# Performance work log

Hardware: AMD Instinct MI355X
Metric: run time of the kernel (lower is better)

## Reference

```python
import jax, jax.numpy as jnp
import numpy as np

N, E, G = 10000, 40000, 128          # nodes, edges, graphs
NF, EF, H, NH, GD, L = 92, 50, 64, 10, 108, 5  # feat dims, hidden, heads, global dim, layers
EPS = 1e-5

def _lrelu(v):
    return jax.nn.leaky_relu(v, 0.2)

def setup_inputs() -> dict:
    key = jax.random.key(0)
    ks = jax.random.split(key, 24)
    def rn(k, shp, s=0.05):
        return jax.random.normal(k, shp, jnp.float32) * s
    return {
        "x": jax.random.normal(ks[0], (N, NF), jnp.float32),
        "edge_index": jax.random.randint(ks[1], (2, E), 0, N, dtype=jnp.int32),
        "edge_attr": jax.random.normal(ks[2], (E, EF), jnp.float32),
        "batch_idx": jnp.sort(jax.random.randint(ks[3], (N,), 0, G, dtype=jnp.int32)),
        "global_features": jax.random.normal(ks[4], (G, GD), jnp.float32),
        "node_W": rn(ks[5], (NF, H)), "node_b": jnp.zeros((H,), jnp.float32),
        "edge_W": rn(ks[6], (EF, H)), "edge_b": jnp.zeros((H,), jnp.float32),
        "conv_W": rn(ks[7], (L, 2 * H, NH * H)),
        "conv_att": rn(ks[8], (L, NH, 2 * H)),
        "conv_b": jnp.zeros((L, H), jnp.float32),
        "conv_gamma": jnp.ones((L, NH), jnp.float32),
        "conv_beta": jnp.zeros((L, NH), jnp.float32),
        "ga_W1": rn(ks[9], (H + GD, H)), "ga_b1": jnp.zeros((H,), jnp.float32),
        "ga_W2": rn(ks[10], (H, 1)), "ga_b2": jnp.zeros((1,), jnp.float32),
        "out_W1": rn(ks[11], (H, H)), "out_b1": jnp.zeros((H,), jnp.float32),
        "out_W2": rn(ks[12], (H, 1)), "out_b2": jnp.zeros((1,), jnp.float32),
    }

def reference(x, edge_index, edge_attr, batch_idx, global_features,
              node_W, node_b, edge_W, edge_b,
              conv_W, conv_att, conv_b, conv_gamma, conv_beta,
              ga_W1, ga_b1, ga_W2, ga_b2, out_W1, out_b1, out_W2, out_b2):
    row, col = edge_index[0], edge_index[1]
    # embeddings
    h = _lrelu(x @ node_W + node_b)            # [N, H]
    ea = _lrelu(edge_attr @ edge_W + edge_b)   # [E, H]
    initial = h
    inv_std = 1.0 / jnp.sqrt(1.0 + EPS)        # DiffGroupNorm eval: running mean=0, var=1
    for i in range(L):
        xi = jnp.concatenate([h[row], ea], axis=-1)               # [E, 2H]
        xj = jnp.concatenate([h[col], ea], axis=-1)
        hi = _lrelu(xi @ conv_W[i]).reshape(E, NH, H)             # [E, NH, H]
        hj = _lrelu(xj @ conv_W[i]).reshape(E, NH, H)
        alpha = jnp.sum(jnp.concatenate([hi, hj], -1) * conv_att[i][None], -1)  # [E, NH]
        alpha = _lrelu(alpha)
        alpha = alpha * inv_std * conv_gamma[i] + conv_beta[i]
        alpha = jax.nn.softmax(alpha, axis=1)                     # softmax over heads
        msg = (hj * alpha[..., None]).reshape(E, NH * H)
        agg = jax.ops.segment_sum(msg, row, num_segments=N).reshape(N, NH, H)
        h_new = agg.mean(axis=1) + conv_b[i]
        h = h + h_new if i > 0 else h_new
    h = h + initial
    # global attention: softmax over nodes within each graph
    g = global_features[batch_idx]                                 # [N, GD]
    s = _lrelu(jnp.concatenate([h, g], -1) @ ga_W1 + ga_b1)
    score = (s @ ga_W2 + ga_b2)[:, 0]                              # [N]
    smax = jax.ops.segment_max(score, batch_idx, num_segments=G)
    ex = jnp.exp(score - smax[batch_idx])
    denom = jax.ops.segment_sum(ex, batch_idx, num_segments=G)
    w = (ex / denom[batch_idx])[:, None]
    h = h * w
    pooled = jax.ops.segment_sum(h, batch_idx, num_segments=G)     # [G, H]
    out = jax.nn.relu(pooled @ out_W1 + out_b1) @ out_W2 + out_b2
    return out[:, 0]
```

## Files before the change

### kernel.cpp

```cpp
#include <hip/hip_runtime.h>
#include <hip/hip_bf16.h>

#define LRELU(v) ((v) > 0.f ? (v) : 0.2f * (v))

__global__ __launch_bounds__(256) void embed_kernel(
    const float* __restrict__ X, const float* __restrict__ W,
    const float* __restrict__ b, float* __restrict__ out, int M, int K) {
  int lane = threadIdx.x & 63;
  int r = blockIdx.x * 4 + (threadIdx.x >> 6);
  if (r >= M) return;
  float acc = b[lane];
  const float* Xr = X + (size_t)r * K;
  for (int k = 0; k < K; ++k) acc = fmaf(Xr[k], W[(size_t)k * 64 + lane], acc);
  acc = LRELU(acc);
  out[(size_t)r * 64 + lane] = acc;
}

template <int ROWS>
__global__ __launch_bounds__(256) void gemm_k64_kernel(
    const float* __restrict__ A, const float* __restrict__ W,
    float* __restrict__ C, int M) {
  const int lane = threadIdx.x & 63;
  const int r0 = (blockIdx.x * 4 + (threadIdx.x >> 6)) * ROWS;
  if (r0 >= M) return;
  float acc[ROWS][10];
#pragma unroll
  for (int r = 0; r < ROWS; ++r)
#pragma unroll
    for (int h = 0; h < 10; ++h) acc[r][h] = 0.f;
  const float* Arow = A + (size_t)r0 * 64;
  for (int k = 0; k < 64; ++k) {
    float w[10];
#pragma unroll
    for (int h = 0; h < 10; ++h) w[h] = W[(size_t)k * 640 + h * 64 + lane];
    float a[ROWS];
#pragma unroll
    for (int r = 0; r < ROWS; ++r) a[r] = Arow[r * 64 + k];
#pragma unroll
    for (int r = 0; r < ROWS; ++r)
#pragma unroll
      for (int h = 0; h < 10; ++h) acc[r][h] = fmaf(a[r], w[h], acc[r][h]);
  }
#pragma unroll
  for (int r = 0; r < ROWS; ++r) {
    float* Crow = C + (size_t)(r0 + r) * 640;
#pragma unroll
    for (int h = 0; h < 10; ++h) Crow[h * 64 + lane] = acc[r][h];
  }
}

__global__ __launch_bounds__(256) void edge_fused_kernel(
    const float* __restrict__ P, const float* __restrict__ ea,
    const float* __restrict__ Wbot,
    const int* __restrict__ row, const int* __restrict__ col,
    const float* __restrict__ att, const float* __restrict__ gamma,
    const float* __restrict__ beta, float* __restrict__ agg, int E_) {
  const int lane = threadIdx.x & 63;
  const int wv = blockIdx.x * 4 + (threadIdx.x >> 6);
  const int e0 = wv * 8;
  if (e0 >= E_) return;

  float eareg[8];
#pragma unroll
  for (int r = 0; r < 8; ++r) {
    int e = e0 + r < E_ ? e0 + r : E_ - 1;
    eareg[r] = ea[(size_t)e * 64 + lane];
  }

  float qacc[8][10];
#pragma unroll
  for (int r = 0; r < 8; ++r)
#pragma unroll
    for (int h = 0; h < 10; ++h) qacc[r][h] = 0.f;
  for (int k = 0; k < 64; ++k) {
    float w[10];
#pragma unroll
    for (int h = 0; h < 10; ++h) w[h] = Wbot[k * 640 + h * 64 + lane];
    float a[8];
#pragma unroll
    for (int r = 0; r < 8; ++r) a[r] = __shfl(eareg[r], k);
#pragma unroll
    for (int r = 0; r < 8; ++r)
#pragma unroll
      for (int h = 0; h < 10; ++h) qacc[r][h] = fmaf(a[r], w[h], qacc[r][h]);
  }

  const float inv_std = 0.9999950000374997f;
#pragma unroll
  for (int r = 0; r < 8; ++r) {
    int e = e0 + r;
    if (e >= E_) break;
    int ri = row[e], ci = col[e];
    const float* Pr = P + (size_t)ri * 640;
    const float* Pc = P + (size_t)ci * 640;
    float hj[10], val[10];
#pragma unroll
    for (int h = 0; h < 10; ++h) {
      float q = qacc[r][h];
      float hi = Pr[h * 64 + lane] + q;
      float hjv = Pc[h * 64 + lane] + q;
      hi = LRELU(hi);
      hjv = LRELU(hjv);
      hj[h] = hjv;
      val[h] = fmaf(hi, att[h * 128 + lane], hjv * att[h * 128 + 64 + lane]);
    }
#pragma unroll
    for (int h = 0; h < 10; ++h) {
      float v = val[h];
#pragma unroll
      for (int off = 32; off; off >>= 1) v += __shfl_xor(v, off);
      val[h] = v;
    }
    float mx = -1e30f;
#pragma unroll
    for (int h = 0; h < 10; ++h) {
      float a = val[h];
      a = LRELU(a);
      a = fmaf(a * inv_std, gamma[h], beta[h]);
      val[h] = a;
      mx = fmaxf(mx, a);
    }
    float ssum = 0.f;
#pragma unroll
    for (int h = 0; h < 10; ++h) {
      float ex = __expf(val[h] - mx);
      val[h] = ex;
      ssum += ex;
    }
    float inv = 1.0f / ssum;
    float m = 0.f;
#pragma unroll
    for (int h = 0; h < 10; ++h) m = fmaf(val[h] * inv, hj[h], m);
    atomicAdd(agg + (size_t)ri * 64 + lane, m);
  }
}

__global__ __launch_bounds__(256) void finalize_kernel(
    float* __restrict__ h, const float* __restrict__ agg,
    const float* __restrict__ b, const float* __restrict__ h0, int mode,
    int total) {
  int idx = blockIdx.x * 256 + threadIdx.x;
  if (idx >= total) return;
  int f = idx & 63;
  float v = fmaf(agg[idx], 0.1f, b[f]);
  if (mode >= 1) v += h[idx];
  if (mode == 2) v += h0[idx];
  h[idx] = v;
}

__global__ __launch_bounds__(256) void score_kernel(
    const float* __restrict__ h, const int* __restrict__ batch,
    const float* __restrict__ gf, const float* __restrict__ W1,
    const float* __restrict__ b1, const float* __restrict__ W2,
    const float* __restrict__ b2, float* __restrict__ score, int N_) {
  int lane = threadIdx.x & 63;
  int n = blockIdx.x * 4 + (threadIdx.x >> 6);
  if (n >= N_) return;
  float acc = b1[lane];
  const float* hn = h + (size_t)n * 64;
#pragma unroll 8
  for (int k = 0; k < 64; ++k) acc = fmaf(hn[k], W1[k * 64 + lane], acc);
  const float* g = gf + (size_t)batch[n] * 108;
#pragma unroll 4
  for (int k = 0; k < 108; ++k) acc = fmaf(g[k], W1[(64 + k) * 64 + lane], acc);
  acc = LRELU(acc);
  float v = acc * W2[lane];
#pragma unroll
  for (int off = 32; off; off >>= 1) v += __shfl_xor(v, off);
  if (lane == 0) score[n] = v + b2[0];
}

__global__ void bounds_kernel(const int* __restrict__ batch,
                              int* __restrict__ start, int N_, int G_) {
  int n = blockIdx.x * blockDim.x + threadIdx.x;
  if (n >= N_) return;
  int b = batch[n];
  int bp = (n == 0) ? -1 : batch[n - 1];
  for (int g = bp + 1; g <= b; ++g) start[g] = n;
  if (n == N_ - 1)
    for (int g = b + 1; g <= G_; ++g) start[g] = N_;
}

__global__ __launch_bounds__(256) void pool_out_kernel(
    const float* __restrict__ h, const float* __restrict__ score,
    const int* __restrict__ start, const float* __restrict__ W1,
    const float* __restrict__ b1, const float* __restrict__ W2,
    const float* __restrict__ b2, float* __restrict__ out) {
  int g = blockIdx.x;
  int s0 = start[g], s1 = start[g + 1];
  int tid = threadIdx.x;
  __shared__ float red[256];
  __shared__ float pool[64];
  __shared__ float sh_smax, sh_denom;
  float lm = -1e30f;
  for (int n = s0 + tid; n < s1; n += 256) lm = fmaxf(lm, score[n]);
  red[tid] = lm;
  __syncthreads();
  for (int off = 128; off; off >>= 1) {
    if (tid < off) red[tid] = fmaxf(red[tid], red[tid + off]);
    __syncthreads();
  }
  if (tid == 0) sh_smax = red[0];
  __syncthreads();
  float smax = sh_smax;
  __syncthreads();
  float ls = 0.f;
  for (int n = s0 + tid; n < s1; n += 256) ls += __expf(score[n] - smax);
  red[tid] = ls;
  __syncthreads();
  for (int off = 128; off; off >>= 1) {
    if (tid < off) red[tid] += red[tid + off];
    __syncthreads();
  }
  if (tid == 0) sh_denom = red[0];
  __syncthreads();
  float denom = sh_denom;
  float invd = denom > 0.f ? 1.0f / denom : 0.f;
  __syncthreads();
  int f = tid & 63, sub = tid >> 6;
  float acc = 0.f;
  for (int n = s0 + sub; n < s1; n += 4)
    acc = fmaf(__expf(score[n] - smax), h[(size_t)n * 64 + f], acc);
  red[tid] = acc;
  __syncthreads();
  if (tid < 64)
    pool[tid] = (red[tid] + red[tid + 64] + red[tid + 128] + red[tid + 192]) * invd;
  __syncthreads();
  if (tid < 64) {
    float a = b1[tid];
#pragma unroll 8
    for (int k = 0; k < 64; ++k) a = fmaf(pool[k], W1[k * 64 + tid], a);
    a = fmaxf(a, 0.f);
    red[tid] = a * W2[tid];
  }
  __syncthreads();
  if (tid == 0) {
    float s = 0.f;
    for (int k = 0; k < 64; ++k) s += red[k];
    out[g] = s + b2[0];
  }
}

extern "C" void kernel_launch(void* const* d_in, const int* in_sizes, int n_in,
                              void* d_out, int out_size, void* d_ws,
                              size_t ws_size, hipStream_t stream) {
  const float* x          = (const float*)d_in[0];
  const int*   edge_index = (const int*)d_in[1];
  const float* edge_attr  = (const float*)d_in[2];
  const int*   batch_idx  = (const int*)d_in[3];
  const float* gf         = (const float*)d_in[4];
  const float* node_W     = (const float*)d_in[5];
  const float* node_b     = (const float*)d_in[6];
  const float* edge_W     = (const float*)d_in[7];
  const float* edge_b     = (const float*)d_in[8];
  const float* conv_W     = (const float*)d_in[9];
  const float* conv_att   = (const float*)d_in[10];
  const float* conv_b     = (const float*)d_in[11];
  const float* conv_gamma = (const float*)d_in[12];
  const float* conv_beta  = (const float*)d_in[13];
  const float* ga_W1      = (const float*)d_in[14];
  const float* ga_b1      = (const float*)d_in[15];
  const float* ga_W2      = (const float*)d_in[16];
  const float* ga_b2      = (const float*)d_in[17];
  const float* out_W1     = (const float*)d_in[18];
  const float* out_b1     = (const float*)d_in[19];
  const float* out_W2     = (const float*)d_in[20];
  const float* out_b2     = (const float*)d_in[21];
  float* out = (float*)d_out;

  const int N = in_sizes[3];
  const int E = in_sizes[2] / 50;
  const int G = in_sizes[4] / 108;
  const int L = 5;

  float* ws = (float*)d_ws;
  float* h    = ws;  ws += (size_t)N * 64;
  float* h0   = ws;  ws += (size_t)N * 64;
  float* ea   = ws;  ws += (size_t)E * 64;
  float* P    = ws;  ws += (size_t)N * 640;
  float* agg  = ws;  ws += (size_t)N * 64;
  float* scr  = ws;  ws += N;
  int* gstart = (int*)ws;

  const int* row = edge_index;
  const int* col = edge_index + E;

  embed_kernel<<<(N + 3) / 4, 256, 0, stream>>>(x, node_W, node_b, h0, N, 92);
  embed_kernel<<<(E + 3) / 4, 256, 0, stream>>>(edge_attr, edge_W, edge_b, ea, E, 50);

  for (int i = 0; i < L; ++i) {
    const float* Wi = conv_W + (size_t)i * 128 * 640;
    gemm_k64_kernel<4><<<(N / 4 + 3) / 4, 256, 0, stream>>>(i == 0 ? h0 : h, Wi, P, N);
    hipMemsetAsync(agg, 0, (size_t)N * 64 * sizeof(float), stream);
    int waves = (E + 7) / 8;
    edge_fused_kernel<<<(waves + 3) / 4, 256, 0, stream>>>(
        P, ea, Wi + 64 * 640, row, col, conv_att + (size_t)i * 1280,
        conv_gamma + i * 10, conv_beta + i * 10, agg, E);
    int mode = (i == 0) ? 0 : (i == L - 1 ? 2 : 1);
    finalize_kernel<<<(N * 64 + 255) / 256, 256, 0, stream>>>(
        h, agg, conv_b + i * 64, h0, mode, N * 64);
  }

  score_kernel<<<(N + 3) / 4, 256, 0, stream>>>(h, batch_idx, gf, ga_W1, ga_b1,
                                                ga_W2, ga_b2, scr, N);
  bounds_kernel<<<(N + 255) / 256, 256, 0, stream>>>(batch_idx, gstart, N, G);
  pool_out_kernel<<<G, 256, 0, stream>>>(h, scr, gstart, out_W1, out_b1, out_W2,
                                         out_b2, out);
}
```

Measured before the change: 849.2 us.

## Sort edges by destination row to reuse row loads and batch atomics

Adds a counting sort of edges by row (histogram, single-block scan, atomic scatter), then permutes the edge embeddings into sorted order once. The fused edge kernel now reuses the source-row projection when consecutive edges share a row, and accumulates messages in a register so it issues one atomic per row run instead of one per edge. Attention weights are hoisted into registers. This adds several setup kernels and an extra E×64 buffer. The scatter order within a row is nondeterministic, so the order of floating-point accumulation can vary between runs.

```diff
diff --git a/kernel.cpp b/kernel.cpp
--- a/kernel.cpp
+++ b/kernel.cpp
@@ -49,22 +49,82 @@
   }
 }
 
+__global__ void hist_kernel(const int* __restrict__ row, int* __restrict__ hist,
+                            int E_) {
+  int e = blockIdx.x * 256 + threadIdx.x;
+  if (e < E_) atomicAdd(&hist[row[e]], 1);
+}
+
+__global__ __launch_bounds__(256) void scan_kernel(int* __restrict__ hist,
+                                                   int* __restrict__ cursor,
+                                                   int NB) {
+  __shared__ int sums[256];
+  int t = threadIdx.x;
+  int chunk = (NB + 255) / 256;
+  int s0 = t * chunk;
+  int local = 0;
+  for (int j = 0; j < chunk; ++j) {
+    int i = s0 + j;
+    if (i < NB) local += hist[i];
+  }
+  sums[t] = local;
+  __syncthreads();
+  for (int off = 1; off < 256; off <<= 1) {
+    int add = (t >= off) ? sums[t - off] : 0;
+    __syncthreads();
+    sums[t] += add;
+    __syncthreads();
+  }
+  int run = (t == 0) ? 0 : sums[t - 1];
+  for (int j = 0; j < chunk; ++j) {
+    int i = s0 + j;
+    if (i < NB) {
+      int v = hist[i];
+      hist[i] = run;
+      cursor[i] = run;
+      run += v;
+    }
+  }
+}
+
+__global__ void scatter_kernel(const int* __restrict__ row,
+                               const int* __restrict__ col,
+                               int* __restrict__ cursor, int* __restrict__ perm,
+                               int* __restrict__ srow, int* __restrict__ scol,
+                               int E_) {
+  int e = blockIdx.x * 256 + threadIdx.x;
+  if (e >= E_) return;
+  int r = row[e];
+  int pos = atomicAdd(&cursor[r], 1);
+  perm[pos] = e;
+  srow[pos] = r;
+  scol[pos] = col[e];
+}
+
+__global__ __launch_bounds__(256) void permute_ea_kernel(
+    const float* __restrict__ ea, const int* __restrict__ perm,
+    float* __restrict__ ea_s, int E_) {
+  int lane = threadIdx.x & 63;
+  int p = blockIdx.x * 4 + (threadIdx.x >> 6);
+  if (p >= E_) return;
+  ea_s[(size_t)p * 64 + lane] = ea[(size_t)perm[p] * 64 + lane];
+}
+
 __global__ __launch_bounds__(256) void edge_fused_kernel(
-    const float* __restrict__ P, const float* __restrict__ ea,
+    const float* __restrict__ P, const float* __restrict__ ea_s,
     const float* __restrict__ Wbot,
-    const int* __restrict__ row, const int* __restrict__ col,
+    const int* __restrict__ srow, const int* __restrict__ scol,
     const float* __restrict__ att, const float* __restrict__ gamma,
     const float* __restrict__ beta, float* __restrict__ agg, int E_) {
   const int lane = threadIdx.x & 63;
-  const int wv = blockIdx.x * 4 + (threadIdx.x >> 6);
-  const int e0 = wv * 8;
+  const int e0 = (blockIdx.x * 4 + (threadIdx.x >> 6)) * 8;
   if (e0 >= E_) return;
 
   float eareg[8];
 #pragma unroll
   for (int r = 0; r < 8; ++r) {
     int e = e0 + r < E_ ? e0 + r : E_ - 1;
-    eareg[r] = ea[(size_t)e * 64 + lane];
+    eareg[r] = ea_s[(size_t)e * 64 + lane];
   }
 
   float qacc[8][10];
@@ -85,24 +145,40 @@
       for (int h = 0; h < 10; ++h) qacc[r][h] = fmaf(a[r], w[h], qacc[r][h]);
   }
 
+  float att1[10], att2[10];
+#pragma unroll
+  for (int h = 0; h < 10; ++h) {
+    att1[h] = att[h * 128 + lane];
+    att2[h] = att[h * 128 + 64 + lane];
+  }
+
   const float inv_std = 0.9999950000374997f;
+  float pr[10];
+  int curRow = -1;
+  float macc = 0.f;
+  int prev = srow[e0];
 #pragma unroll
   for (int r = 0; r < 8; ++r) {
     int e = e0 + r;
     if (e >= E_) break;
-    int ri = row[e], ci = col[e];
-    const float* Pr = P + (size_t)ri * 640;
+    int ri = srow[e], ci = scol[e];
+    if (ri != curRow) {
+      curRow = ri;
+      const float* Pr = P + (size_t)ri * 640;
+#pragma unroll
+      for (int h = 0; h < 10; ++h) pr[h] = Pr[h * 64 + lane];
+    }
     const float* Pc = P + (size_t)ci * 640;
     float hj[10], val[10];
 #pragma unroll
     for (int h = 0; h < 10; ++h) {
       float q = qacc[r][h];
-      float hi = Pr[h * 64 + lane] + q;
+      float hi = pr[h] + q;
       float hjv = Pc[h * 64 + lane] + q;
       hi = LRELU(hi);
       hjv = LRELU(hjv);
       hj[h] = hjv;
-      val[h] = fmaf(hi, att[h * 128 + lane], hjv * att[h * 128 + 64 + lane]);
+      val[h] = fmaf(hi, att1[h], hjv * att2[h]);
     }
 #pragma unroll
     for (int h = 0; h < 10; ++h) {
@@ -131,8 +207,14 @@
     float m = 0.f;
 #pragma unroll
     for (int h = 0; h < 10; ++h) m = fmaf(val[h] * inv, hj[h], m);
-    atomicAdd(agg + (size_t)ri * 64 + lane, m);
-  }
+    if (ri != prev) {
+      atomicAdd(agg + (size_t)prev * 64 + lane, macc);
+      macc = 0.f;
+      prev = ri;
+    }
+    macc += m;
+  }
+  atomicAdd(agg + (size_t)prev * 64 + lane, macc);
 }
 
 __global__ __launch_bounds__(256) void finalize_kernel(
@@ -277,16 +359,29 @@
   float* h    = ws;  ws += (size_t)N * 64;
   float* h0   = ws;  ws += (size_t)N * 64;
   float* ea   = ws;  ws += (size_t)E * 64;
+  float* ea_s = ws;  ws += (size_t)E * 64;
   float* P    = ws;  ws += (size_t)N * 640;
   float* agg  = ws;  ws += (size_t)N * 64;
   float* scr  = ws;  ws += N;
-  int* gstart = (int*)ws;
+  int* gstart = (int*)ws;  ws += G + 2;
+  int* hist   = (int*)ws;  ws += N;
+  int* cursor = (int*)ws;  ws += N;
+  int* perm   = (int*)ws;  ws += E;
+  int* srow   = (int*)ws;  ws += E;
+  int* scol   = (int*)ws;  ws += E;
 
   const int* row = edge_index;
   const int* col = edge_index + E;
 
+  hipMemsetAsync(hist, 0, (size_t)N * sizeof(int), stream);
+  hist_kernel<<<(E + 255) / 256, 256, 0, stream>>>(row, hist, E);
+  scan_kernel<<<1, 256, 0, stream>>>(hist, cursor, N);
+  scatter_kernel<<<(E + 255) / 256, 256, 0, stream>>>(row, col, cursor, perm,
+                                                      srow, scol, E);
+
   embed_kernel<<<(N + 3) / 4, 256, 0, stream>>>(x, node_W, node_b, h0, N, 92);
   embed_kernel<<<(E + 3) / 4, 256, 0, stream>>>(edge_attr, edge_W, edge_b, ea, E, 50);
+  permute_ea_kernel<<<(E + 3) / 4, 256, 0, stream>>>(ea, perm, ea_s, E);
 
   for (int i = 0; i < L; ++i) {
     const float* Wi = conv_W + (size_t)i * 128 * 640;
@@ -294,7 +389,7 @@
     hipMemsetAsync(agg, 0, (size_t)N * 64 * sizeof(float), stream);
     int waves = (E + 7) / 8;
     edge_fused_kernel<<<(waves + 3) / 4, 256, 0, stream>>>(
-        P, ea, Wi + 64 * 640, row, col, conv_att + (size_t)i * 1280,
+        P, ea_s, Wi + 64 * 640, srow, scol, conv_att + (size_t)i * 1280,
         conv_gamma + i * 10, conv_beta + i * 10, agg, E);
     int mode = (i == 0) ? 0 : (i == L - 1 ? 2 : 1);
     finalize_kernel<<<(N * 64 + 255) / 256, 256, 0, stream>>>(
```

Result: slower. 897.2 us (+5.6%).
